# Kernel optimization log

Measured on AMD Instinct MI355X. Metric: run time of the kernel, lower is better.

The kernel has to match this reference:

```python
import jax, jax.numpy as jnp
import numpy as np
from jax import lax

D_MODEL = 2048
D_STATE = 16
D_CONV = 4
B_SZ = 2
T_LEN = 2048


def setup_inputs() -> dict:
    key = jax.random.key(0)
    ks = jax.random.split(key, 8)
    x = jax.random.normal(ks[0], (B_SZ, T_LEN, D_MODEL), dtype=jnp.float32)
    h = jnp.zeros((B_SZ, D_MODEL, D_STATE), dtype=jnp.float32)
    norm_w = jnp.ones((D_MODEL,), dtype=jnp.float32)
    in_proj_w = jax.random.normal(ks[1], (2 * D_MODEL, D_MODEL), dtype=jnp.float32) * (D_MODEL ** -0.5)
    conv_w = jax.random.normal(ks[2], (D_MODEL, 1, D_CONV), dtype=jnp.float32) * 0.5
    conv_b = jnp.zeros((D_MODEL,), dtype=jnp.float32)
    x_proj_w = jax.random.normal(ks[3], (D_MODEL + 2 * D_STATE, D_MODEL), dtype=jnp.float32) * (D_MODEL ** -0.5)
    A_log = jnp.broadcast_to(jnp.log(jnp.arange(1, D_STATE + 1, dtype=jnp.float32))[None, :], (D_MODEL, D_STATE)).copy()
    D = jnp.ones((D_MODEL,), dtype=jnp.float32)
    out_proj_w = jax.random.normal(ks[4], (D_MODEL, D_MODEL), dtype=jnp.float32) * (D_MODEL ** -0.5)
    return {"x": x, "h": h, "norm_w": norm_w, "in_proj_w": in_proj_w,
            "conv_w": conv_w, "conv_b": conv_b, "x_proj_w": x_proj_w,
            "A_log": A_log, "D": D, "out_proj_w": out_proj_w}


def _rmsnorm(x, w, eps=1e-6):
    ms = jnp.mean(jnp.square(x.astype(jnp.float32)), axis=-1, keepdims=True)
    return (x * lax.rsqrt(ms + eps).astype(x.dtype)) * w.astype(x.dtype)


def reference(x, h, norm_w, in_proj_w, conv_w, conv_b, x_proj_w, A_log, D, out_proj_w):
    B, T, d_model = x.shape
    d_state = A_log.shape[1]
    residual = x
    x_normed = _rmsnorm(x, norm_w)
    xz = x_normed @ in_proj_w.T                      # (B, T, 2*d_model)
    x_branch, z = jnp.split(xz, 2, axis=-1)
    # depthwise causal conv1d: torch pads both sides by d_conv-1 then slices [:T],
    # equivalent to left-pad-only causal conv.
    xc = x_branch.transpose(0, 2, 1)                 # (B, d_model, T)
    xc = lax.conv_general_dilated(
        xc, conv_w, window_strides=(1,), padding=[(D_CONV - 1, 0)],
        dimension_numbers=("NCH", "OIH", "NCH"), feature_group_count=d_model)
    xc = xc + conv_b[None, :, None]
    x_ssm = jax.nn.silu(xc.transpose(0, 2, 1))       # (B, T, d_model)

    # SSM core
    proj = x_ssm @ x_proj_w.T                        # (B, T, d_model + 2*d_state)
    delta_raw = proj[..., :d_model]
    B_in = proj[..., d_model:d_model + d_state]
    C_in = proj[..., d_model + d_state:]
    delta = jax.nn.softplus(delta_raw)               # (B, T, d_model)
    A = -jnp.exp(A_log.astype(jnp.float32))          # (d_model, d_state)

    def step(h_c, inp):
        d_t, b_t, c_t, x_t = inp                     # (B,dm) (B,ds) (B,ds) (B,dm)
        A_bar = jnp.exp(d_t[:, :, None] * A[None])   # (B, dm, ds)
        h_c = A_bar * h_c + (d_t * x_t)[:, :, None] * b_t[:, None, :]
        y_t = jnp.einsum("bdn,bn->bd", h_c, c_t) + D * x_t
        return h_c, y_t

    xs = (delta.transpose(1, 0, 2), B_in.transpose(1, 0, 2),
          C_in.transpose(1, 0, 2), x_ssm.transpose(1, 0, 2))
    h_new, ys = lax.scan(step, h.astype(x.dtype), xs)
    y = ys.transpose(1, 0, 2)                        # (B, T, d_model)

    y = y * jax.nn.silu(z)
    out = residual + y @ out_proj_w.T
    return out, lax.stop_gradient(h_new)
```

## Files before the change

kernel.cpp:

```cpp
#include <hip/hip_runtime.h>
#include <cstdint>
#include <cstddef>


typedef __bf16 bf16_t;
typedef __attribute__((ext_vector_type(8))) __bf16 bf16x8;
typedef __attribute__((ext_vector_type(4))) __bf16 bf16x4;
typedef __attribute__((ext_vector_type(4))) float f32x4;

#define D_MODEL 2048
#define D_STATE 16
#define B_SZ 2
#define T_LEN 2048
#define N_ROWS (B_SZ * T_LEN)
#define N_PAD  2304
#define N_CHUNK 32
#define L_CHUNK (T_LEN / N_CHUNK)
#define LOG2E 1.4426950408889634f

__device__ __forceinline__ void load_lds16(const void* g, void* l) {
    __builtin_amdgcn_global_load_lds(
        (const __attribute__((address_space(1))) void*)(uintptr_t)g,
        (__attribute__((address_space(3))) void*)(uintptr_t)l,
        16, 0, 0);
}

#define VMW(n) asm volatile("s_waitcnt vmcnt(" #n ")" ::: "memory")
#define BARG() do { __builtin_amdgcn_s_barrier(); __builtin_amdgcn_sched_barrier(0); } while (0)

__global__ __launch_bounds__(256) void cast_w13(
    const float* __restrict__ w1, const float* __restrict__ w3,
    bf16_t* __restrict__ d1, bf16_t* __restrict__ d3)
{
    int i = blockIdx.x * 256 + threadIdx.x;
    const int n1 = 4096 * 2048 / 4;
    if (i < n1) {
        f32x4 v = ((const f32x4*)w1)[i];
        ((bf16x4*)d1)[i] = __builtin_convertvector(v, bf16x4);
    } else {
        int j = i - n1;
        f32x4 v = ((const f32x4*)w3)[j];
        ((bf16x4*)d3)[j] = __builtin_convertvector(v, bf16x4);
    }
}

__global__ __launch_bounds__(256) void cast_pad_w2(
    const float* __restrict__ s, bf16_t* __restrict__ d)
{
    int i = blockIdx.x * 256 + threadIdx.x;
    int row = i >> 11;
    int col = i & 2047;
    float v = (row < 2080) ? s[(size_t)row * 2048 + col] : 0.f;
    d[i] = (bf16_t)v;
}

__global__ __launch_bounds__(256) void rmsnorm_kernel(
    const float* __restrict__ x, const float* __restrict__ w,
    bf16_t* __restrict__ xn)
{
    int row = blockIdx.x;
    int tid = threadIdx.x;
    const f32x4* xr = (const f32x4*)(x + (size_t)row * D_MODEL);
    f32x4 v0 = xr[tid];
    f32x4 v1 = xr[tid + 256];
    float ss = 0.f;
    #pragma unroll
    for (int e = 0; e < 4; ++e) { ss = fmaf(v0[e], v0[e], ss); ss = fmaf(v1[e], v1[e], ss); }
    #pragma unroll
    for (int o = 32; o > 0; o >>= 1) ss += __shfl_down(ss, o, 64);
    __shared__ float red[4];
    if ((tid & 63) == 0) red[tid >> 6] = ss;
    __syncthreads();
    float tot = red[0] + red[1] + red[2] + red[3];
    float scale = rsqrtf(tot * (1.f / D_MODEL) + 1e-6f);
    const f32x4* w4 = (const f32x4*)w;
    f32x4 m0 = v0 * w4[tid] * scale;
    f32x4 m1 = v1 * w4[tid + 256] * scale;
    bf16x4* xo = (bf16x4*)(xn + (size_t)row * D_MODEL);
    xo[tid]       = __builtin_convertvector(m0, bf16x4);
    xo[tid + 256] = __builtin_convertvector(m1, bf16x4);
}

template<int MODE>
__global__ __launch_bounds__(512, 2) void gemm_bt(
    const bf16_t* __restrict__ A, const bf16_t* __restrict__ Bw, int K,
    float* __restrict__ out0, bf16_t* __restrict__ out1,
    const float* __restrict__ add)
{
    __shared__ __align__(16) char smem[131072];
    char* const ldsAp = smem;
    char* const ldsBp = smem + 32768;

    const int tid  = threadIdx.x;
    const int nwg = gridDim.x * gridDim.y;
    const int lin = blockIdx.x + gridDim.x * blockIdx.y;
    const int wg  = (lin & 7) * (nwg >> 3) + (lin >> 3);
    const int bm  = wg & 15;
    const int bn  = wg >> 4;

    const int lane = tid & 63;
    const int wave = tid >> 6;
    const int wm   = wave >> 2;
    const int wn   = wave & 3;
    const int fr   = lane & 15;
    const int quad = lane >> 4;

    const int rS   = tid >> 2;
    const int cS   = tid & 3;
    const int gcol = ((cS - ((rS >> 1) & 3)) & 3) * 8;
    const bf16_t* sAn = A  + (size_t)(bm * 256 + rS) * K + gcol;
    const bf16_t* sBn = Bw + (size_t)(bn * 256 + rS) * K + gcol;

    const int swz  = ((quad + ((fr >> 1) & 3)) & 3) * 8;
    const int aOff = (wm * 128 + fr) * 32 + swz;
    const int bOff = (wn * 64  + fr) * 32 + swz;

    f32x4 acc[8][4];
    #pragma unroll
    for (int i = 0; i < 8; ++i)
        #pragma unroll
        for (int j = 0; j < 4; ++j) acc[i][j] = {0.f, 0.f, 0.f, 0.f};

    bf16x8 afr[2][4];
    bf16x8 bfr[2][4];

#define STG_A(b, s) do { \
        char* l_ = ldsAp + (b) * 65536 + (s) * 16384 + tid * 16; \
        load_lds16(sAn, l_); load_lds16(sAn + (size_t)128 * K, l_ + 8192); \
        sAn += 32; } while (0)
#define STG_B(b, s) do { \
        char* l_ = ldsBp + (b) * 65536 + (s) * 16384 + tid * 16; \
        load_lds16(sBn, l_); load_lds16(sBn + (size_t)128 * K, l_ + 8192); \
        sBn += 32; } while (0)

#define MFMA16(MIH, MAB, MBB)                                                 \
    __builtin_amdgcn_s_setprio(1);                                            \
    _Pragma("unroll")                                                         \
    for (int i = 0; i < 4; ++i)                                               \
        _Pragma("unroll")                                                     \
        for (int j = 0; j < 4; ++j)                                           \
            acc[(MIH)*4+i][j] = __builtin_amdgcn_mfma_f32_16x16x32_bf16(      \
                afr[MAB][i], bfr[MBB][j], acc[(MIH)*4+i][j], 0, 0, 0);        \
    __builtin_amdgcn_s_setprio(0);

#define RD_A(RBUF, RS, RIH, RAB) {                                            \
    const bf16_t* pA_ = (const bf16_t*)(ldsAp + (RBUF)*65536 + (RS)*16384);   \
    _Pragma("unroll")                                                         \
    for (int i = 0; i < 4; ++i)                                               \
        afr[RAB][i] = *(const bf16x8*)(pA_ + aOff + ((RIH)*4+i)*512); }

#define RD_B(RBUF, RS, RBB) {                                                 \
    const bf16_t* pB_ = (const bf16_t*)(ldsBp + (RBUF)*65536 + (RS)*16384);   \
    _Pragma("unroll")                                                         \
    for (int j = 0; j < 4; ++j)                                               \
        bfr[RBB][j] = *(const bf16x8*)(pB_ + bOff + j*512); }

    STG_B(0, 0); STG_A(0, 0); STG_B(0, 1); STG_A(0, 1);
    STG_B(1, 0); STG_A(1, 0); STG_B(1, 1);
    VMW(6); BARG();
    RD_B(0, 0, 0) RD_A(0, 0, 0, 0)

    const int NI = K >> 7;
    for (int I = 0; I < NI - 1; ++I) {
        STG_A(1,1); RD_A(0,0,1,1) MFMA16(0,0,0)                  BARG();
        STG_B(0,0); RD_B(0,1,1) RD_A(0,1,0,0) MFMA16(1,1,0) VMW(4); BARG();
        STG_A(0,0); RD_A(0,1,1,1) MFMA16(0,0,1)                  BARG();
        STG_B(0,1); RD_B(1,0,0) RD_A(1,0,0,0) MFMA16(1,1,1) VMW(4); BARG();
        STG_A(0,1); RD_A(1,0,1,1) MFMA16(0,0,0)                  BARG();
        STG_B(1,0); RD_B(1,1,1) RD_A(1,1,0,0) MFMA16(1,1,0) VMW(4); BARG();
        STG_A(1,0); RD_A(1,1,1,1) MFMA16(0,0,1)                  BARG();
        STG_B(1,1); RD_B(0,0,0) RD_A(0,0,0,0) MFMA16(1,1,1) VMW(4); BARG();
    }
    STG_A(1,1); RD_A(0,0,1,1) MFMA16(0,0,0)              BARG();
    RD_B(0,1,1) RD_A(0,1,0,0) MFMA16(1,1,0)      VMW(4); BARG();
    RD_A(0,1,1,1) MFMA16(0,0,1)                          BARG();
    RD_B(1,0,0) RD_A(1,0,0,0) MFMA16(1,1,1)      VMW(0); BARG();
    RD_A(1,0,1,1) MFMA16(0,0,0)                          BARG();
    RD_B(1,1,1) RD_A(1,1,0,0) MFMA16(1,1,0)              BARG();
    RD_A(1,1,1,1) MFMA16(0,0,1)                          BARG();
    MFMA16(1,1,1)
#undef STG_A
#undef STG_B
#undef MFMA16
#undef RD_A
#undef RD_B

    float* const cs = (float*)smem;
    __syncthreads();
    #pragma unroll
    for (int s = 0; s < 4; ++s) {
        if (wm == (s >> 1)) {
            #pragma unroll
            for (int ii = 0; ii < 4; ++ii)
                #pragma unroll
                for (int j = 0; j < 4; ++j)
                    #pragma unroll
                    for (int rr = 0; rr < 4; ++rr)
                        cs[(ii * 16 + quad * 4 + rr) * 268 + wn * 64 + j * 16 + fr]
                            = acc[(s & 1) * 4 + ii][j][rr];
        }
        __syncthreads();
        #pragma unroll
        for (int k = 0; k < 8; ++k) {
            const int idx = tid + k * 512;
            const int row = idx >> 6;
            const int c4  = (idx & 63) << 2;
            f32x4 v = *(const f32x4*)(cs + row * 268 + c4);
            const int gr = bm * 256 + s * 64 + row;
            const int gc = bn * 256 + c4;
            if (MODE == 0) {
                if (bn < 8) {
                    *(f32x4*)&out0[(size_t)gr * 2048 + gc] = v;
                } else {
                    bf16x4 o;
                    #pragma unroll
                    for (int e = 0; e < 4; ++e) {
                        float sv = v[e];
                        o[e] = (bf16_t)(sv / (1.f + __expf(-sv)));
                    }
                    *(bf16x4*)&out1[(size_t)gr * 2048 + (gc - 2048)] = o;
                }
            } else if (MODE == 1) {
                if (bn < 8) {
                    #pragma unroll
                    for (int e = 0; e < 4; ++e) {
                        float sv = v[e];
                        v[e] = fmaxf(sv, 0.f) + __logf(1.f + __expf(-fabsf(sv)));
                    }
                }
                *(f32x4*)&out0[(size_t)gr * N_PAD + gc] = v;
            } else {
                f32x4 a4 = *(const f32x4*)&add[(size_t)gr * 2048 + gc];
                *(f32x4*)&out0[(size_t)gr * 2048 + gc] = v + a4;
            }
        }
        __syncthreads();
    }
}

__global__ __launch_bounds__(256) void conv_silu_kernel(
    const float* __restrict__ xb, const float* __restrict__ cw,
    const float* __restrict__ cb, bf16_t* __restrict__ xs_b)
{
    int id = blockIdx.x * 256 + threadIdx.x;
    int d  = id & 2047;
    int tb = (id >> 11) & 255;
    int b  = id >> 19;
    float w0 = cw[d * 4 + 0], w1 = cw[d * 4 + 1], w2 = cw[d * 4 + 2], w3 = cw[d * 4 + 3];
    float bias = cb[d];
    int t0 = tb * 8;
    size_t base = (size_t)b * T_LEN;
    float v[11];
    #pragma unroll
    for (int i = 0; i < 11; ++i) {
        int t = t0 - 3 + i;
        v[i] = (t >= 0) ? xb[(base + t) * 2048 + d] : 0.f;
    }
    #pragma unroll
    for (int j = 0; j < 8; ++j) {
        float s = bias + w0 * v[j] + w1 * v[j + 1] + w2 * v[j + 2] + w3 * v[j + 3];
        float sl = s / (1.f + __expf(-s));
        xs_b[(base + t0 + j) * D_MODEL + d] = (bf16_t)sl;
    }
}

#define PF 4

__global__ __launch_bounds__(256) void scan_phase1(
    const float* __restrict__ proj, const bf16_t* __restrict__ xs,
    const float* __restrict__ A_log,
    float* __restrict__ Aprod, float* __restrict__ hfin)
{
    const int wiu  = __builtin_amdgcn_readfirstlane(
                         blockIdx.x * 4 + (threadIdx.x >> 6));
    const int lane = threadIdx.x & 63;
    const int nq   = lane & 3;
    const int dsub = lane >> 2;
    const int c  = wiu & 31;
    const int dg = (wiu >> 5) & 127;
    const int b  = wiu >> 12;
    const int dd = dg * 16 + dsub;

    float A2[4], h[4];
    #pragma unroll
    for (int j = 0; j < 4; ++j) {
        A2[j] = -__expf(A_log[dd * D_STATE + nq * 4 + j]) * LOG2E;
        h[j] = 0.f;
    }
    float sda = 0.f;

    const int t0 = c * L_CHUNK;
    const float*  pr = proj + (size_t)(b * T_LEN + t0) * N_PAD;
    const bf16_t* px = xs   + (size_t)(b * T_LEN + t0) * D_MODEL;
    const int offB = D_MODEL + nq * 4;

    float p_da[PF], p_xv[PF];
    f32x4 p_B[PF];
    #pragma unroll
    for (int u = 0; u < PF; ++u) {
        p_da[u] = pr[dd];
        p_B[u]  = *(const f32x4*)(pr + offB);
        p_xv[u] = (float)px[dd];
        pr += N_PAD; px += D_MODEL;
    }
    for (int g = 0; g < L_CHUNK / PF - 1; ++g) {
        #pragma unroll
        for (int u = 0; u < PF; ++u) {
            float da = p_da[u], xv = p_xv[u];
            f32x4 Bv = p_B[u];
            p_da[u] = pr[dd];
            p_B[u]  = *(const f32x4*)(pr + offB);
            p_xv[u] = (float)px[dd];
            pr += N_PAD; px += D_MODEL;
            float dx = da * xv;
            sda += da;
            #pragma unroll
            for (int j = 0; j < 4; ++j) {
                float a = exp2f(da * A2[j]);
                h[j] = fmaf(a, h[j], dx * Bv[j]);
            }
        }
    }
    #pragma unroll
    for (int u = 0; u < PF; ++u) {
        float da = p_da[u], xv = p_xv[u];
        f32x4 Bv = p_B[u];
        float dx = da * xv;
        sda += da;
        #pragma unroll
        for (int j = 0; j < 4; ++j) {
            float a = exp2f(da * A2[j]);
            h[j] = fmaf(a, h[j], dx * Bv[j]);
        }
    }
    size_t o = ((size_t)c * 4096 + b * 2048 + dd) * D_STATE + nq * 4;
    *(f32x4*)(Aprod + o) = f32x4{exp2f(A2[0] * sda), exp2f(A2[1] * sda),
                                 exp2f(A2[2] * sda), exp2f(A2[3] * sda)};
    *(f32x4*)(hfin  + o) = f32x4{h[0], h[1], h[2], h[3]};
}

__global__ __launch_bounds__(256) void scan_phase2(
    const float* __restrict__ h_in, const float* __restrict__ Aprod,
    float* __restrict__ hfin, float* __restrict__ h_out)
{
    int g = blockIdx.x * 256 + threadIdx.x;
    float h = h_in[g];
    for (int c = 0; c < N_CHUNK; ++c) {
        size_t o = (size_t)c * 65536 + g;
        float a   = Aprod[o];
        float loc = hfin[o];
        hfin[o] = h;
        h = fmaf(a, h, loc);
    }
    h_out[g] = h;
}

__global__ __launch_bounds__(256) void scan_phase3(
    const float* __restrict__ proj, const bf16_t* __restrict__ xs,
    const bf16_t* __restrict__ zg, const float* __restrict__ A_log,
    const float* __restrict__ Dv, const float* __restrict__ hinit,
    bf16_t* __restrict__ yg)
{
    const int wiu  = __builtin_amdgcn_readfirstlane(
                         blockIdx.x * 4 + (threadIdx.x >> 6));
    const int lane = threadIdx.x & 63;
    const int nq   = lane & 3;
    const int dsub = lane >> 2;
    const int c  = wiu & 31;
    const int dg = (wiu >> 5) & 127;
    const int b  = wiu >> 12;
    const int dd = dg * 16 + dsub;

    float A2[4], h[4];
    size_t o = ((size_t)c * 4096 + b * 2048 + dd) * D_STATE + nq * 4;
    #pragma unroll
    for (int j = 0; j < 4; ++j) {
        A2[j] = -__expf(A_log[dd * D_STATE + nq * 4 + j]) * LOG2E;
        h[j]  = hinit[o + j];
    }
    float Dd = Dv[dd];

    const int t0 = c * L_CHUNK;
    const float*  pr = proj + (size_t)(b * T_LEN + t0) * N_PAD;
    const bf16_t* px = xs   + (size_t)(b * T_LEN + t0) * D_MODEL;
    const bf16_t* pz = zg   + (size_t)(b * T_LEN + t0) * 2048;
    bf16_t*       py = yg   + (size_t)(b * T_LEN + t0) * D_MODEL;
    const int offB = D_MODEL + nq * 4;
    const int offC = D_MODEL + D_STATE + nq * 4;

    float p_da[PF], p_xv[PF], p_sz[PF];
    f32x4 p_B[PF], p_C[PF];
    #pragma unroll
    for (int u = 0; u < PF; ++u) {
        p_da[u] = pr[dd];
        p_B[u]  = *(const f32x4*)(pr + offB);
        p_C[u]  = *(const f32x4*)(pr + offC);
        p_xv[u] = (float)px[dd];
        p_sz[u] = (float)pz[dd];
        pr += N_PAD; px += D_MODEL; pz += 2048;
    }

#define P3_STEP(da, xv, sz, Bv, Cv)                                       \
    {                                                                     \
        float dx = da * xv;                                               \
        float yp = 0.f;                                                   \
        _Pragma("unroll")                                                 \
        for (int j = 0; j < 4; ++j) {                                     \
            float a = exp2f(da * A2[j]);                                  \
            h[j] = fmaf(a, h[j], dx * Bv[j]);                             \
            yp = fmaf(h[j], Cv[j], yp);                                   \
        }                                                                 \
        yp += __shfl_xor(yp, 1, 64);                                      \
        yp += __shfl_xor(yp, 2, 64);                                      \
        if (nq == 0) {                                                    \
            float y = fmaf(Dd, xv, yp);                                   \
            py[dd] = (bf16_t)(y * sz);                                    \
        }                                                                 \
        py += D_MODEL;                                                    \
    }

    for (int g = 0; g < L_CHUNK / PF - 1; ++g) {
        #pragma unroll
        for (int u = 0; u < PF; ++u) {
            float da = p_da[u], xv = p_xv[u], sz = p_sz[u];
            f32x4 Bv = p_B[u], Cv = p_C[u];
            p_da[u] = pr[dd];
            p_B[u]  = *(const f32x4*)(pr + offB);
            p_C[u]  = *(const f32x4*)(pr + offC);
            p_xv[u] = (float)px[dd];
            p_sz[u] = (float)pz[dd];
            pr += N_PAD; px += D_MODEL; pz += 2048;
            P3_STEP(da, xv, sz, Bv, Cv)
        }
    }
    #pragma unroll
    for (int u = 0; u < PF; ++u) {
        float da = p_da[u], xv = p_xv[u], sz = p_sz[u];
        f32x4 Bv = p_B[u], Cv = p_C[u];
        P3_STEP(da, xv, sz, Bv, Cv)
    }
#undef P3_STEP
}

extern "C" void kernel_launch(void* const* d_in, const int* in_sizes, int n_in,
                              void* d_out, int out_size, void* d_ws, size_t ws_size,
                              hipStream_t stream)
{
    const float* x    = (const float*)d_in[0];
    const float* h0   = (const float*)d_in[1];
    const float* nw   = (const float*)d_in[2];
    const float* w_in = (const float*)d_in[3];
    const float* cw   = (const float*)d_in[4];
    const float* cb   = (const float*)d_in[5];
    const float* w_x  = (const float*)d_in[6];
    const float* alog = (const float*)d_in[7];
    const float* dv   = (const float*)d_in[8];
    const float* w_out= (const float*)d_in[9];
    float* out  = (float*)d_out;
    float* hout = out + (size_t)N_ROWS * D_MODEL;

    char* ws = (char*)d_ws;
    size_t off = 0;
    auto alloc = [&](size_t bytes) -> void* {
        void* p = ws + off;
        off += (bytes + 255) & ~(size_t)255;
        return p;
    };
    bf16_t* W1  = (bf16_t*)alloc((size_t)4096 * 2048 * 2);
    bf16_t* W2  = (bf16_t*)alloc((size_t)N_PAD * 2048 * 2);
    bf16_t* W3  = (bf16_t*)alloc((size_t)2048 * 2048 * 2);
    bf16_t* XN  = (bf16_t*)alloc((size_t)N_ROWS * 2048 * 2);
    float*  XB  = (float*) alloc((size_t)N_ROWS * 2048 * 4);
    bf16_t* ZG  = (bf16_t*)alloc((size_t)N_ROWS * 2048 * 2);
    float*  PROJ= (float*) alloc((size_t)N_ROWS * N_PAD * 4);
    float* APROD= (float*) alloc((size_t)N_CHUNK * 4096 * D_STATE * 4);
    float* HFIN = (float*) alloc((size_t)N_CHUNK * 4096 * D_STATE * 4);
    bf16_t* XSb = W1;
    bf16_t* YG  = XN;

    cast_w13<<<(4096 * 2048 / 4 + 2048 * 2048 / 4) / 256, 256, 0, stream>>>(w_in, w_out, W1, W3);
    cast_pad_w2<<<(N_PAD * 2048) / 256, 256, 0, stream>>>(w_x, W2);

    rmsnorm_kernel<<<N_ROWS, 256, 0, stream>>>(x, nw, XN);
    gemm_bt<0><<<dim3(16, 16), 512, 0, stream>>>(XN, W1, 2048, XB, ZG, nullptr);
    conv_silu_kernel<<<(B_SZ * (T_LEN / 8) * D_MODEL) / 256, 256, 0, stream>>>(XB, cw, cb, XSb);
    gemm_bt<1><<<dim3(16, N_PAD / 256), 512, 0, stream>>>(XSb, W2, 2048, PROJ, nullptr, nullptr);
    scan_phase1<<<2048, 256, 0, stream>>>(PROJ, XSb, alog, APROD, HFIN);
    scan_phase2<<<256, 256, 0, stream>>>(h0, APROD, HFIN, hout);
    scan_phase3<<<2048, 256, 0, stream>>>(PROJ, XSb, ZG, alog, dv, HFIN, YG);
    gemm_bt<2><<<dim3(16, 8), 512, 0, stream>>>(YG, W3, 2048, out, nullptr, x);

    (void)in_sizes; (void)n_in; (void)out_size; (void)ws_size;
}
```

Baseline: 466.3 us.

## Use smaller 128x128 GEMM tiles for x_proj and out_proj, shrink padding

Adds a simpler 128x128-tile GEMM kernel, used for the x_proj and out_proj projections in place of the 256x256 pipelined kernel. Those GEMMs now launch more workgroups (512 instead of 128 for out_proj), which fills more of the chip's compute units. The x_proj output padding drops from 2304 to 2176 columns, cutting wasted columns and memory traffic. The scan also gets a deeper prefetch (PF 4 to 8) and a DPP-based quad reduction instead of shuffles. The trade-off is that the new GEMM has a single-buffered LDS loop with no prefetch overlap, so it may hide latency worse than the old pipelined kernel.

Measured after the change: 462.5 us. Within noise of the previous version (-0.8%).

```diff
diff --git a/kernel.cpp b/kernel.cpp
--- a/kernel.cpp
+++ b/kernel.cpp
@@ -13,7 +13,7 @@
 #define B_SZ 2
 #define T_LEN 2048
 #define N_ROWS (B_SZ * T_LEN)
-#define N_PAD  2304
+#define N_PAD  2176
 #define N_CHUNK 32
 #define L_CHUNK (T_LEN / N_CHUNK)
 #define LOG2E 1.4426950408889634f
@@ -27,6 +27,16 @@
 
 #define VMW(n) asm volatile("s_waitcnt vmcnt(" #n ")" ::: "memory")
 #define BARG() do { __builtin_amdgcn_s_barrier(); __builtin_amdgcn_sched_barrier(0); } while (0)
+
+__device__ __forceinline__ float quad_add(float v) {
+    int t = __builtin_amdgcn_mov_dpp(__builtin_bit_cast(int, v),
+                                     0xB1, 0xF, 0xF, true);
+    v += __builtin_bit_cast(float, t);
+    t = __builtin_amdgcn_mov_dpp(__builtin_bit_cast(int, v),
+                                 0x4E, 0xF, 0xF, true);
+    v += __builtin_bit_cast(float, t);
+    return v;
+}
 
 __global__ __launch_bounds__(256) void cast_w13(
     const float* __restrict__ w1, const float* __restrict__ w3,
@@ -81,11 +91,9 @@
     xo[tid + 256] = __builtin_convertvector(m1, bf16x4);
 }
 
-template<int MODE>
 __global__ __launch_bounds__(512, 2) void gemm_bt(
     const bf16_t* __restrict__ A, const bf16_t* __restrict__ Bw, int K,
-    float* __restrict__ out0, bf16_t* __restrict__ out1,
-    const float* __restrict__ add)
+    float* __restrict__ out0, bf16_t* __restrict__ out1)
 {
     __shared__ __align__(16) char smem[131072];
     char* const ldsAp = smem;
@@ -132,7 +140,6 @@
         char* l_ = ldsBp + (b) * 65536 + (s) * 16384 + tid * 16; \
         load_lds16(sBn, l_); load_lds16(sBn + (size_t)128 * K, l_ + 8192); \
         sBn += 32; } while (0)
-
 #define MFMA16(MIH, MAB, MBB)                                                 \
     __builtin_amdgcn_s_setprio(1);                                            \
     _Pragma("unroll")                                                         \
@@ -142,13 +149,11 @@
             acc[(MIH)*4+i][j] = __builtin_amdgcn_mfma_f32_16x16x32_bf16(      \
                 afr[MAB][i], bfr[MBB][j], acc[(MIH)*4+i][j], 0, 0, 0);        \
     __builtin_amdgcn_s_setprio(0);
-
 #define RD_A(RBUF, RS, RIH, RAB) {                                            \
     const bf16_t* pA_ = (const bf16_t*)(ldsAp + (RBUF)*65536 + (RS)*16384);   \
     _Pragma("unroll")                                                         \
     for (int i = 0; i < 4; ++i)                                               \
         afr[RAB][i] = *(const bf16x8*)(pA_ + aOff + ((RIH)*4+i)*512); }
-
 #define RD_B(RBUF, RS, RBB) {                                                 \
     const bf16_t* pB_ = (const bf16_t*)(ldsBp + (RBUF)*65536 + (RS)*16384);   \
     _Pragma("unroll")                                                         \
@@ -208,24 +213,110 @@
             f32x4 v = *(const f32x4*)(cs + row * 268 + c4);
             const int gr = bm * 256 + s * 64 + row;
             const int gc = bn * 256 + c4;
-            if (MODE == 0) {
-                if (bn < 8) {
-                    *(f32x4*)&out0[(size_t)gr * 2048 + gc] = v;
-                } else {
-                    bf16x4 o;
+            if (bn < 8) {
+                *(f32x4*)&out0[(size_t)gr * 2048 + gc] = v;
+            } else {
+                bf16x4 o;
+                #pragma unroll
+                for (int e = 0; e < 4; ++e) {
+                    float sv = v[e];
+                    o[e] = (bf16_t)(sv / (1.f + __expf(-sv)));
+                }
+                *(bf16x4*)&out1[(size_t)gr * 2048 + (gc - 2048)] = o;
+            }
+        }
+        __syncthreads();
+    }
+}
+
+template<int MODE>
+__global__ __launch_bounds__(256, 2) void gemm128(
+    const bf16_t* __restrict__ A, const bf16_t* __restrict__ Bw, int K,
+    float* __restrict__ out0, const float* __restrict__ add)
+{
+    __shared__ __align__(16) bf16_t lA[128 * 32];
+    __shared__ __align__(16) bf16_t lB[128 * 32];
+    __shared__ __align__(16) float  cs[32 * 132];
+
+    const int tid = threadIdx.x;
+    const int nwg = gridDim.x * gridDim.y;
+    const int lin = blockIdx.x + gridDim.x * blockIdx.y;
+    const int wg  = (lin & 7) * (nwg >> 3) + (lin >> 3);
+    const int bm  = wg & 31;
+    const int bn  = wg >> 5;
+
+    const int lane = tid & 63;
+    const int wave = tid >> 6;
+    const int wm   = wave & 1;
+    const int wn   = wave >> 1;
+    const int fr   = lane & 15;
+    const int quad = lane >> 4;
+
+    const int rS   = tid >> 2;
+    const int cS   = tid & 3;
+    const int gcol = ((cS - ((rS >> 1) & 3)) & 3) * 8;
+    const bf16_t* sA = A  + (size_t)(bm * 128 + rS) * K + gcol;
+    const bf16_t* sB = Bw + (size_t)(bn * 128 + rS) * K + gcol;
+
+    const int swz  = ((quad + ((fr >> 1) & 3)) & 3) * 8;
+    const int aOff = (wm * 64 + fr) * 32 + swz;
+    const int bOff = (wn * 64 + fr) * 32 + swz;
+
+    f32x4 acc[4][4];
+    #pragma unroll
+    for (int i = 0; i < 4; ++i)
+        #pragma unroll
+        for (int j = 0; j < 4; ++j) acc[i][j] = {0.f, 0.f, 0.f, 0.f};
+
+    const int nt = K >> 5;
+    for (int kt = 0; kt < nt; ++kt) {
+        load_lds16(sA,                 (char*)lA + tid * 16);
+        load_lds16(sA + (size_t)64 * K,(char*)lA + 4096 + tid * 16);
+        load_lds16(sB,                 (char*)lB + tid * 16);
+        load_lds16(sB + (size_t)64 * K,(char*)lB + 4096 + tid * 16);
+        sA += 32; sB += 32;
+        __syncthreads();
+
+        bf16x8 af[4], bv[4];
+        #pragma unroll
+        for (int i = 0; i < 4; ++i) af[i] = *(const bf16x8*)(lA + aOff + i * 512);
+        #pragma unroll
+        for (int j = 0; j < 4; ++j) bv[j] = *(const bf16x8*)(lB + bOff + j * 512);
+        __builtin_amdgcn_s_setprio(1);
+        #pragma unroll
+        for (int i = 0; i < 4; ++i)
+            #pragma unroll
+            for (int j = 0; j < 4; ++j)
+                acc[i][j] = __builtin_amdgcn_mfma_f32_16x16x32_bf16(
+                    af[i], bv[j], acc[i][j], 0, 0, 0);
+        __builtin_amdgcn_s_setprio(0);
+        __syncthreads();
+    }
+
+    const int lrow0 = wm * 16 + quad * 4;
+    const int lcol0 = wn * 64 + fr;
+    for (int i = 0; i < 4; ++i) {
+        __syncthreads();
+        #pragma unroll
+        for (int j = 0; j < 4; ++j)
+            #pragma unroll
+            for (int rr = 0; rr < 4; ++rr)
+                cs[(lrow0 + rr) * 132 + lcol0 + j * 16] = acc[i][j][rr];
+        __syncthreads();
+        #pragma unroll
+        for (int k = 0; k < 4; ++k) {
+            int f4  = tid + k * 256;
+            int row = f4 >> 5;
+            int c4  = (f4 & 31) * 4;
+            f32x4 v = *(const f32x4*)&cs[row * 132 + c4];
+            int gr = bm * 128 + i * 16 + ((row < 16) ? row : (48 + row));
+            int gc = bn * 128 + c4;
+            if (MODE == 1) {
+                if (bn < 16) {
                     #pragma unroll
                     for (int e = 0; e < 4; ++e) {
-                        float sv = v[e];
-                        o[e] = (bf16_t)(sv / (1.f + __expf(-sv)));
-                    }
-                    *(bf16x4*)&out1[(size_t)gr * 2048 + (gc - 2048)] = o;
-                }
-            } else if (MODE == 1) {
-                if (bn < 8) {
-                    #pragma unroll
-                    for (int e = 0; e < 4; ++e) {
-                        float sv = v[e];
-                        v[e] = fmaxf(sv, 0.f) + __logf(1.f + __expf(-fabsf(sv)));
+                        float s = v[e];
+                        v[e] = fmaxf(s, 0.f) + __logf(1.f + __expf(-fabsf(s)));
                     }
                 }
                 *(f32x4*)&out0[(size_t)gr * N_PAD + gc] = v;
@@ -234,7 +325,6 @@
                 *(f32x4*)&out0[(size_t)gr * 2048 + gc] = v + a4;
             }
         }
-        __syncthreads();
     }
 }
 
@@ -264,7 +354,7 @@
     }
 }
 
-#define PF 4
+#define PF 8
 
 __global__ __launch_bounds__(256) void scan_phase1(
     const float* __restrict__ proj, const bf16_t* __restrict__ xs,
@@ -410,8 +500,7 @@
             h[j] = fmaf(a, h[j], dx * Bv[j]);                             \
             yp = fmaf(h[j], Cv[j], yp);                                   \
         }                                                                 \
-        yp += __shfl_xor(yp, 1, 64);                                      \
-        yp += __shfl_xor(yp, 2, 64);                                      \
+        yp = quad_add(yp);                                                \
         if (nq == 0) {                                                    \
             float y = fmaf(Dd, xv, yp);                                   \
             py[dd] = (bf16_t)(y * sz);                                    \
@@ -482,13 +571,13 @@
     cast_pad_w2<<<(N_PAD * 2048) / 256, 256, 0, stream>>>(w_x, W2);
 
     rmsnorm_kernel<<<N_ROWS, 256, 0, stream>>>(x, nw, XN);
-    gemm_bt<0><<<dim3(16, 16), 512, 0, stream>>>(XN, W1, 2048, XB, ZG, nullptr);
+    gemm_bt<<<dim3(16, 16), 512, 0, stream>>>(XN, W1, 2048, XB, ZG);
     conv_silu_kernel<<<(B_SZ * (T_LEN / 8) * D_MODEL) / 256, 256, 0, stream>>>(XB, cw, cb, XSb);
-    gemm_bt<1><<<dim3(16, N_PAD / 256), 512, 0, stream>>>(XSb, W2, 2048, PROJ, nullptr, nullptr);
+    gemm128<1><<<dim3(32, N_PAD / 128), 256, 0, stream>>>(XSb, W2, 2048, PROJ, nullptr);
     scan_phase1<<<2048, 256, 0, stream>>>(PROJ, XSb, alog, APROD, HFIN);
     scan_phase2<<<256, 256, 0, stream>>>(h0, APROD, HFIN, hout);
     scan_phase3<<<2048, 256, 0, stream>>>(PROJ, XSb, ZG, alog, dv, HFIN, YG);
-    gemm_bt<2><<<dim3(16, 8), 512, 0, stream>>>(YG, W3, 2048, out, nullptr, x);
+    gemm128<2><<<dim3(32, 16), 256, 0, stream>>>(YG, W3, 2048, out, x);
 
     (void)in_sizes; (void)n_in; (void)out_size; (void)ws_size;
 }
```
